# Kernel tuning notes

Measured on AMD Instinct MI355X. Metric: run time of the kernel, lower is better.

Reference implementation:

```python
import jax, jax.numpy as jnp
import numpy as np

CHUNK = 64
L2_EPS = 1e-6
RMS_EPS = 1e-5


def _silu(x):
    return x * jax.nn.sigmoid(x)


def _causal_shared_conv(x, w):
    # x: [B,T,C]; w: [K] single kernel shared across all channels (depthwise).
    K = w.shape[0]
    T = x.shape[1]
    xp = jnp.pad(x, ((0, 0), (K - 1, 0), (0, 0)))
    out = w[0] * xp[:, 0:T, :]
    for j in range(1, K):  # K=4, tiny fixed loop
        out = out + w[j] * xp[:, j:j + T, :]
    return out


def _l2norm(x):
    return x * jax.lax.rsqrt(jnp.sum(x * x, axis=-1, keepdims=True) + L2_EPS)


def _delta_rule_chunk(q, k, v, beta, chunk=CHUNK):
    # q,k: [B,H,T,dk]; v: [B,H,T,dv]; beta: [B,H,T]
    B, H, T, dk = q.shape
    dv = v.shape[-1]
    q = q * (dk ** -0.5)
    nC = T // chunk
    q = q.reshape(B, H, nC, chunk, dk)
    k = k.reshape(B, H, nC, chunk, dk)
    v = v.reshape(B, H, nC, chunk, dv)
    beta = beta.reshape(B, H, nC, chunk)
    k_beta = k * beta[..., None]
    v_beta = v * beta[..., None]
    # UT transform: invert the unit-lower-triangular (I + stril(K_beta K^T))
    A = jnp.einsum('bhncd,bhnmd->bhncm', k_beta, k)  # [B,H,nC,C,C]
    stril = jnp.tril(jnp.ones((chunk, chunk), bool), -1)
    M = jnp.where(stril, A, 0.0) + jnp.eye(chunk, dtype=q.dtype)
    u = jax.scipy.linalg.solve_triangular(M, v_beta, lower=True)  # T @ (beta*v)
    w = jax.scipy.linalg.solve_triangular(M, k_beta, lower=True)  # T @ (beta*k)
    tril_incl = jnp.tril(jnp.ones((chunk, chunk), bool))

    def step(S, inp):
        q_i, k_i, u_i, w_i = inp  # [B,H,C,d*]
        u_i = u_i - jnp.einsum('bhcd,bhde->bhce', w_i, S)
        attn = jnp.where(tril_incl, jnp.einsum('bhcd,bhmd->bhcm', q_i, k_i), 0.0)
        o_i = jnp.einsum('bhcd,bhde->bhce', q_i, S) + jnp.einsum('bhcm,bhme->bhce', attn, u_i)
        S = S + jnp.einsum('bhcd,bhce->bhde', k_i, u_i)
        return S, o_i

    xs = tuple(jnp.moveaxis(t, 2, 0) for t in (q, k, u, w))
    S0 = jnp.zeros((B, H, dk, dv), q.dtype)
    _, o = jax.lax.scan(step, S0, xs)  # o: [nC,B,H,C,dv]
    return jnp.moveaxis(o, 0, 2).reshape(B, H, T, dv)


def setup_inputs() -> dict:
    key = jax.random.key(0)
    ks = jax.random.split(key, 10)
    B, T, D, H = 2, 4096, 2048, 16
    sc = 0.02
    return {
        'x': jax.random.normal(ks[0], (B, T, D), jnp.float32),
        'Wq': jax.random.normal(ks[1], (D, D), jnp.float32) * sc,
        'Wk': jax.random.normal(ks[2], (D, D), jnp.float32) * sc,
        'Wv': jax.random.normal(ks[3], (D, D), jnp.float32) * sc,
        'Wb': jax.random.normal(ks[4], (D, H), jnp.float32) * sc,
        'Wo': jax.random.normal(ks[5], (D, D), jnp.float32) * sc,
        'conv_q': jax.random.normal(ks[6], (4,), jnp.float32) * 0.5,
        'conv_k': jax.random.normal(ks[7], (4,), jnp.float32) * 0.5,
        'conv_v': jax.random.normal(ks[8], (4,), jnp.float32) * 0.5,
        'onorm_w': jnp.ones((D // H,), jnp.float32),
    }


def reference(x, Wq, Wk, Wv, Wb, Wo, conv_q, conv_k, conv_v, onorm_w):
    B, T, D = x.shape
    H = Wb.shape[1]
    dk = Wq.shape[1] // H
    dv = Wv.shape[1] // H
    # projections + shared-kernel causal short conv (silu activation)
    q = _silu(_causal_shared_conv(x @ Wq, conv_q))
    k = _silu(_causal_shared_conv(x @ Wk, conv_k))
    v = _silu(_causal_shared_conv(x @ Wv, conv_v))
    beta = jax.nn.sigmoid(x @ Wb)  # [B,T,H]
    # split heads -> [B,H,T,d]
    qh = _l2norm(q.reshape(B, T, H, dk)).transpose(0, 2, 1, 3)
    kh = _l2norm(k.reshape(B, T, H, dk)).transpose(0, 2, 1, 3)
    vh = v.reshape(B, T, H, dv).transpose(0, 2, 1, 3)
    o = _delta_rule_chunk(qh, kh, vh, beta.transpose(0, 2, 1))  # [B,H,T,dv]
    o = o.transpose(0, 2, 1, 3)  # [B,T,H,dv]
    # per-head RMSNorm over head_v_dim
    o = o * jax.lax.rsqrt(jnp.mean(o * o, axis=-1, keepdims=True) + RMS_EPS) * onorm_w
    return o.reshape(B, T, H * dv) @ Wo
```

## Files before the change

kernel.cpp:

```cpp
#include <hip/hip_runtime.h>
#include <math.h>

#define B_ 2
#define T_ 4096
#define D_ 2048
#define H_ 16
#define DK 128
#define DV 128
#define CH 64
#define M_ (B_ * T_)
#define NCH (T_ / CH)

typedef __attribute__((ext_vector_type(8))) short bfrag;
typedef __attribute__((ext_vector_type(4))) float ffrag;
typedef __attribute__((ext_vector_type(8))) unsigned short u16x8;
typedef unsigned short us;

#define MFMA __builtin_amdgcn_mfma_f32_16x16x32_bf16

__device__ inline us f2bf(float f) {
  union { float f; unsigned u; } v; v.f = f;
  unsigned r = v.u + 0x7fffu + ((v.u >> 16) & 1u);
  return (us)(r >> 16);
}
__device__ inline float bf2f(us u) {
  union { unsigned u; float f; } v; v.u = ((unsigned)u) << 16;
  return v.f;
}

__device__ inline void gl_lds16(const us* g, us* l) {
  __builtin_amdgcn_global_load_lds(
      (const __attribute__((address_space(1))) void*)g,
      (__attribute__((address_space(3))) void*)l, 16, 0, 0);
}

__global__ __launch_bounds__(256) void to_bf16(const float* __restrict__ in,
                                               us* __restrict__ out) {
  const size_t i = ((size_t)blockIdx.x * 256 + threadIdx.x) * 8;
  const float4 a = *reinterpret_cast<const float4*>(in + i);
  const float4 b = *reinterpret_cast<const float4*>(in + i + 4);
  ushort4 o0, o1;
  o0.x = f2bf(a.x); o0.y = f2bf(a.y); o0.z = f2bf(a.z); o0.w = f2bf(a.w);
  o1.x = f2bf(b.x); o1.y = f2bf(b.y); o1.z = f2bf(b.z); o1.w = f2bf(b.w);
  *reinterpret_cast<ushort4*>(out + i) = o0;
  *reinterpret_cast<ushort4*>(out + i + 4) = o1;
}

__global__ __launch_bounds__(256) void wtrans(const float* __restrict__ W,
                                              us* __restrict__ Wt) {
  __shared__ float tile[64][68];
  const int k0 = blockIdx.y * 64, n0 = blockIdx.x * 64;
  const int lr = threadIdx.x >> 4, lc = (threadIdx.x & 15) * 4;
#pragma unroll
  for (int p = 0; p < 4; ++p) {
    const int r = lr + p * 16;
    *reinterpret_cast<float4*>(&tile[r][lc]) =
        *reinterpret_cast<const float4*>(&W[(size_t)(k0 + r) * D_ + n0 + lc]);
  }
  __syncthreads();
#pragma unroll
  for (int p = 0; p < 4; ++p) {
    const int r = lr + p * 16;
    ushort4 o;
    o.x = f2bf(tile[lc + 0][r]); o.y = f2bf(tile[lc + 1][r]);
    o.z = f2bf(tile[lc + 2][r]); o.w = f2bf(tile[lc + 3][r]);
    *reinterpret_cast<ushort4*>(&Wt[(size_t)(n0 + r) * D_ + k0 + lc]) = o;
  }
}

template <bool OUTF32>
__global__ __launch_bounds__(512, 2) void gemm256(const us* __restrict__ A,
                                                  const us* __restrict__ Bt,
                                                  void* __restrict__ Cp,
                                                  int M, int N, int K) {
  __shared__ __align__(16) us lds[2][2][2][256 * 32];
  const int t = threadIdx.x, l = t & 63, w = t >> 6;
  const int wm = w >> 2, wn = w & 3;
  const int fr = l & 15, hi = l >> 4;
  const int sx = 8 * (hi ^ ((fr >> 1) & 3));

  const int m0 = blockIdx.y * 256;
  const int n0 = blockIdx.x * 256;

  const int srow = t >> 2;
  const int scol = 8 * ((t & 3) ^ ((t >> 3) & 3));
  const us* Ab = A + (size_t)(m0 + srow) * K + scol;
  const us* Bb = Bt + (size_t)(n0 + srow) * K + scol;

  ffrag acc[8][4];
#pragma unroll
  for (int mi = 0; mi < 8; ++mi)
#pragma unroll
    for (int ni = 0; ni < 4; ++ni)
#pragma unroll
      for (int e = 0; e < 4; ++e) acc[mi][ni][e] = 0.f;

#define STG_A(bf, kk, kt)                                                      \
  do {                                                                         \
    gl_lds16(Ab + (size_t)(kt) * 64 + (kk) * 32, &lds[bf][0][kk][t * 8]);      \
    gl_lds16(Ab + (size_t)128 * K + (size_t)(kt) * 64 + (kk) * 32,             \
             &lds[bf][0][kk][4096 + t * 8]);                                   \
  } while (0)
#define STG_B(bf, kk, kt)                                                      \
  do {                                                                         \
    gl_lds16(Bb + (size_t)(kt) * 64 + (kk) * 32, &lds[bf][1][kk][t * 8]);      \
    gl_lds16(Bb + (size_t)128 * K + (size_t)(kt) * 64 + (kk) * 32,             \
             &lds[bf][1][kk][4096 + t * 8]);                                   \
  } while (0)

  const int NT = K >> 6;
  STG_A(0, 0, 0); STG_B(0, 0, 0); STG_A(0, 1, 0); STG_B(0, 1, 0);
  asm volatile("s_waitcnt vmcnt(4)" ::: "memory");
  __builtin_amdgcn_s_barrier();
  __builtin_amdgcn_sched_barrier(0);

  const int arow = wm * 128 + fr;
  const int brow = wn * 64 + fr;

#pragma unroll 1
  for (int kt = 0; kt < NT; ++kt) {
    const int cur = kt & 1, oth = cur ^ 1;
    const bool pf = (kt + 1 < NT);
    bfrag af4[4], bf4[4];

    {
      const us* pa = &lds[cur][0][0][0];
      const us* pb = &lds[cur][1][0][0];
#pragma unroll
      for (int ni = 0; ni < 4; ++ni)
        bf4[ni] = *reinterpret_cast<const bfrag*>(pb + (brow + ni * 16) * 32 + sx);
#pragma unroll
      for (int mi = 0; mi < 4; ++mi)
        af4[mi] = *reinterpret_cast<const bfrag*>(pa + (arow + mi * 16) * 32 + sx);
      if (pf) STG_A(oth, 0, kt + 1);
      __builtin_amdgcn_s_setprio(1);
#pragma unroll
      for (int mi = 0; mi < 4; ++mi)
#pragma unroll
        for (int ni = 0; ni < 4; ++ni)
          acc[mi][ni] = MFMA(af4[mi], bf4[ni], acc[mi][ni], 0, 0, 0);
      __builtin_amdgcn_s_setprio(0);
#pragma unroll
      for (int mi = 0; mi < 4; ++mi)
        af4[mi] = *reinterpret_cast<const bfrag*>(pa + (arow + 64 + mi * 16) * 32 + sx);
      if (pf) STG_B(oth, 0, kt + 1);
      __builtin_amdgcn_s_setprio(1);
#pragma unroll
      for (int mi = 0; mi < 4; ++mi)
#pragma unroll
        for (int ni = 0; ni < 4; ++ni)
          acc[mi + 4][ni] = MFMA(af4[mi], bf4[ni], acc[mi + 4][ni], 0, 0, 0);
      __builtin_amdgcn_s_setprio(0);
    }
    if (pf) asm volatile("s_waitcnt vmcnt(4)" ::: "memory");
    else    asm volatile("s_waitcnt vmcnt(0)" ::: "memory");
    __builtin_amdgcn_s_barrier();
    __builtin_amdgcn_sched_barrier(0);

    {
      const us* pa = &lds[cur][0][1][0];
      const us* pb = &lds[cur][1][1][0];
#pragma unroll
      for (int ni = 0; ni < 4; ++ni)
        bf4[ni] = *reinterpret_cast<const bfrag*>(pb + (brow + ni * 16) * 32 + sx);
#pragma unroll
      for (int mi = 0; mi < 4; ++mi)
        af4[mi] = *reinterpret_cast<const bfrag*>(pa + (arow + mi * 16) * 32 + sx);
      if (pf) STG_A(oth, 1, kt + 1);
      __builtin_amdgcn_s_setprio(1);
#pragma unroll
      for (int mi = 0; mi < 4; ++mi)
#pragma unroll
        for (int ni = 0; ni < 4; ++ni)
          acc[mi][ni] = MFMA(af4[mi], bf4[ni], acc[mi][ni], 0, 0, 0);
      __builtin_amdgcn_s_setprio(0);
#pragma unroll
      for (int mi = 0; mi < 4; ++mi)
        af4[mi] = *reinterpret_cast<const bfrag*>(pa + (arow + 64 + mi * 16) * 32 + sx);
      if (pf) STG_B(oth, 1, kt + 1);
      __builtin_amdgcn_s_setprio(1);
#pragma unroll
      for (int mi = 0; mi < 4; ++mi)
#pragma unroll
        for (int ni = 0; ni < 4; ++ni)
          acc[mi + 4][ni] = MFMA(af4[mi], bf4[ni], acc[mi + 4][ni], 0, 0, 0);
      __builtin_amdgcn_s_setprio(0);
    }
    if (pf) asm volatile("s_waitcnt vmcnt(4)" ::: "memory");
    else    asm volatile("s_waitcnt vmcnt(0)" ::: "memory");
    __builtin_amdgcn_s_barrier();
    __builtin_amdgcn_sched_barrier(0);
  }
#undef STG_A
#undef STG_B

  const int crow = m0 + wm * 128 + hi * 4;
  const int ccol = n0 + wn * 64 + fr;
#pragma unroll
  for (int mi = 0; mi < 8; ++mi)
#pragma unroll
    for (int ni = 0; ni < 4; ++ni)
#pragma unroll
      for (int j = 0; j < 4; ++j) {
        const size_t idx = (size_t)(crow + mi * 16 + j) * N + ccol + ni * 16;
        if constexpr (OUTF32) ((float*)Cp)[idx] = acc[mi][ni][j];
        else ((us*)Cp)[idx] = f2bf(acc[mi][ni][j]);
      }
}

__device__ inline void conv_body(const us* __restrict__ in, const float* cw,
                                 int bt, int d0, int mode, float v[8]) {
  const int tb = bt & (T_ - 1);
  const us* row = in + (size_t)bt * D_ + d0;
#pragma unroll
  for (int j = 0; j < 8; ++j) v[j] = 0.f;
#pragma unroll
  for (int j = 0; j < 4; ++j) {
    if (tb >= j) {
      const us* rp = row - (size_t)(j * D_);
      const ushort4 a = *reinterpret_cast<const ushort4*>(rp);
      const ushort4 b = *reinterpret_cast<const ushort4*>(rp + 4);
      const float wj = cw[3 - j];
      v[0] = fmaf(wj, bf2f(a.x), v[0]); v[1] = fmaf(wj, bf2f(a.y), v[1]);
      v[2] = fmaf(wj, bf2f(a.z), v[2]); v[3] = fmaf(wj, bf2f(a.w), v[3]);
      v[4] = fmaf(wj, bf2f(b.x), v[4]); v[5] = fmaf(wj, bf2f(b.y), v[5]);
      v[6] = fmaf(wj, bf2f(b.z), v[6]); v[7] = fmaf(wj, bf2f(b.w), v[7]);
    }
  }
#pragma unroll
  for (int j = 0; j < 8; ++j) v[j] = v[j] / (1.f + expf(-v[j]));
  if (mode) {
    float ss = 0.f;
#pragma unroll
    for (int j = 0; j < 8; ++j) ss = fmaf(v[j], v[j], ss);
    ss += __shfl_xor(ss, 1);
    ss += __shfl_xor(ss, 2);
    ss += __shfl_xor(ss, 4);
    ss += __shfl_xor(ss, 8);
    float sc = rsqrtf(ss + 1e-6f);
    if (mode == 2) sc *= 0.08838834764831845f;
#pragma unroll
    for (int j = 0; j < 8; ++j) v[j] *= sc;
  }
}

__global__ __launch_bounds__(256) void conv_silu_plain(const us* __restrict__ in,
                                                       const float* __restrict__ cw,
                                                       us* __restrict__ out) {
  const int bt = blockIdx.x, d0 = threadIdx.x * 8;
  float v[8];
  conv_body(in, cw, bt, d0, 0, v);
  ushort4 o0, o1;
  o0.x = f2bf(v[0]); o0.y = f2bf(v[1]); o0.z = f2bf(v[2]); o0.w = f2bf(v[3]);
  o1.x = f2bf(v[4]); o1.y = f2bf(v[5]); o1.z = f2bf(v[6]); o1.w = f2bf(v[7]);
  us* op = out + (size_t)bt * D_ + d0;
  *reinterpret_cast<ushort4*>(op) = o0;
  *reinterpret_cast<ushort4*>(op + 4) = o1;
}

__global__ __launch_bounds__(256) void conv_silu_chunk(const us* __restrict__ in,
                                                       const float* __restrict__ cw,
                                                       us* __restrict__ out,
                                                       int mode) {
  const int bt = blockIdx.x, d0 = threadIdx.x * 8;
  float v[8];
  conv_body(in, cw, bt, d0, mode, v);
  const int b = bt >> 12, tt = bt & (T_ - 1);
  const int cid = tt >> 6, r = tt & 63;
  const int h = d0 >> 7, g = (d0 & 127) >> 3;
  us* dst = out + ((size_t)((b * H_ + h) * NCH + cid)) * (CH * DK) +
            r * 128 + ((g ^ (r & 15)) * 8);
  ushort4 o0, o1;
  o0.x = f2bf(v[0]); o0.y = f2bf(v[1]); o0.z = f2bf(v[2]); o0.w = f2bf(v[3]);
  o1.x = f2bf(v[4]); o1.y = f2bf(v[5]); o1.z = f2bf(v[6]); o1.w = f2bf(v[7]);
  *reinterpret_cast<ushort4*>(dst) = o0;
  *reinterpret_cast<ushort4*>(dst + 4) = o1;
}

__global__ __launch_bounds__(256) void beta_sigmoid(const float* __restrict__ x,
                                                    const float* __restrict__ Wb,
                                                    float* __restrict__ betaT) {
  const int t = threadIdx.x;
  const int m = blockIdx.x * 4 + (t >> 6);
  const int l = t & 63;
  const int c = l & 15;
  const int s = l >> 4;
  const float* xr = x + (size_t)m * D_;
  const int kb = s * (D_ / 4);
  float acc = 0.f;
  for (int k = 0; k < D_ / 4; ++k)
    acc = fmaf(xr[kb + k], Wb[(size_t)(kb + k) * H_ + c], acc);
  acc += __shfl_xor(acc, 16);
  acc += __shfl_xor(acc, 32);
  if (l < 16) {
    const int b = m >> 12, tt = m & (T_ - 1);
    betaT[((size_t)(b * H_ + c)) * T_ + tt] = 1.f / (1.f + expf(-acc));
  }
}

__device__ inline void prod_step(float* Tf, const float* Am, float* xbuf,
                                 int r, int c, int I, int J,
                                 int nk, int K0, int K1, int K2) {
  float X = 0.f;
  const int Ks[3] = {K0, K1, K2};
  for (int kk = 0; kk < nk; ++kk) {
    const int K = Ks[kk];
    const float* amrow = Am + (16 * I + r) * 72 + 16 * K;
    const float* tcol = Tf + (16 * K) * 68 + 16 * J + c;
#pragma unroll
    for (int m = 0; m < 16; ++m) X = fmaf(amrow[m], tcol[m * 68], X);
  }
  __syncthreads();
  xbuf[r * 17 + c] = X;
  __syncthreads();
  float s = 0.f;
  const float* trow = Tf + (16 * I + r) * 68 + 16 * I;
#pragma unroll
  for (int m = 0; m < 16; ++m) s = fmaf(trow[m], xbuf[m * 17 + c], s);
  Tf[(16 * I + r) * 68 + 16 * J + c] = -s;
  __syncthreads();
}

__global__ __launch_bounds__(256, 2) void delta_prep(const us* __restrict__ qch,
                                                     const us* __restrict__ kch,
                                                     const float* __restrict__ betaT,
                                                     us* __restrict__ v_uv,
                                                     us* __restrict__ Wout,
                                                     us* __restrict__ kTout,
                                                     us* __restrict__ Aout) {
  __shared__ __align__(16) unsigned char lds[72000];
  us*    ks    = (us*)(lds);
  us*    Tb    = (us*)(lds);
  float* Am    = (float*)(lds + 16384);
  us*    vTb   = (us*)(lds + 16384);
  float* Tf    = (float*)(lds + 34816);
  us*    atst  = (us*)(lds + 34816);
  us*    Wst   = (us*)(lds + 34816);
  us*    kTb   = (us*)(lds + 52224);
  us*    UVst  = (us*)(lds + 52224);
  float* betac = (float*)(lds + 70656);
  float* xbuf  = (float*)(lds + 70912);

  const int t = threadIdx.x, w = t >> 6, l = t & 63;
  const int rr = l & 15, hi = l >> 4;
  const int bx = blockIdx.x;
  const int bh = bx >> 6, cid = bx & 63;
  const int b = bh >> 4, h = bh & 15;
  const size_t rowbase = ((size_t)b * T_ + (size_t)cid * CH) * D_ + (size_t)h * DK;
  const size_t cbase = (size_t)bx * (CH * DK);
  const size_t abase = (size_t)bx * (CH * CH);

  {
    const us* kg = kch + cbase;
#pragma unroll
    for (int p = 0; p < 4; ++p)
      gl_lds16(kg + p * 2048 + t * 8, ks + p * 2048 + t * 8);
    const float4 z = make_float4(0.f, 0.f, 0.f, 0.f);
    *reinterpret_cast<float4*>(atst + t * 16) = z;
    *reinterpret_cast<float4*>(atst + t * 16 + 8) = z;
    if (t < 64) betac[t] = betaT[(size_t)bh * T_ + cid * CH + t];
  }
  __syncthreads();

  {
    bfrag qf[4], kf[4];
#pragma unroll
    for (int k4 = 0; k4 < 4; ++k4) {
      const int go = ((4 * k4 + hi) ^ rr) * 8;
      qf[k4] = *reinterpret_cast<const bfrag*>(qch + cbase + (16 * w + rr) * 128 + go);
      kf[k4] = *reinterpret_cast<const bfrag*>(ks + (16 * w + rr) * 128 + go);
    }
    for (int jt = 0; jt <= w; ++jt) {
      ffrag accA = {0.f, 0.f, 0.f, 0.f}, accQ = {0.f, 0.f, 0.f, 0.f};
#pragma unroll
      for (int k4 = 0; k4 < 4; ++k4) {
        const bfrag bfr = *reinterpret_cast<const bfrag*>(
            ks + (16 * jt + rr) * 128 + (((4 * k4 + hi) ^ rr) * 8));
        accA = MFMA(kf[k4], bfr, accA, 0, 0, 0);
        accQ = MFMA(qf[k4], bfr, accQ, 0, 0, 0);
      }
#pragma unroll
      for (int j4 = 0; j4 < 4; ++j4) {
        const int i = 16 * w + 4 * hi + j4, j = 16 * jt + rr;
        Am[i * 72 + j] = (j < i) ? betac[i] * accA[j4] : 0.f;
        if (j <= i)
          atst[i * 64 + (((j >> 3) ^ (i & 7)) * 8) + (j & 7)] = f2bf(accQ[j4]);
      }
    }
    const int r = t & 63, part = t >> 6;
#pragma unroll
    for (int gi = 0; gi < 4; ++gi) {
      const int g = 4 * part + gi;
      const u16x8 kv = *reinterpret_cast<const u16x8*>(ks + r * 128 + ((g ^ (r & 15)) * 8));
#pragma unroll
      for (int j = 0; j < 8; ++j) kTb[(g * 8 + j) * 72 + r] = kv[j];
    }
  }
  __syncthreads();

  {
#pragma unroll
    for (int p = 0; p < 2; ++p) {
      const int unit = t + p * 256;
      *reinterpret_cast<u16x8*>(Aout + abase + unit * 8) =
          *reinterpret_cast<const u16x8*>(atst + unit * 8);
    }
#pragma unroll
    for (int p = 0; p < 4; ++p) {
      const int unit = t + p * 256;
      const int d = unit >> 3, sg = unit & 7;
      *reinterpret_cast<u16x8*>(kTout + cbase + unit * 8) =
          *reinterpret_cast<const u16x8*>(kTb + d * 72 + ((sg ^ (d & 7)) * 8));
    }
  }
  __syncthreads();
  for (int i = t; i < 64 * 68; i += 256) Tf[i] = 0.f;
  __syncthreads();

  if (t < 64) {
    const int blk = t >> 4, j = t & 15, bd = blk * 16;
    Tf[(bd + j) * 68 + bd + j] = 1.f;
    for (int i = j + 1; i < 16; ++i) {
      float s = 0.f;
      for (int m = j; m < i; ++m)
        s = fmaf(Am[(bd + i) * 72 + bd + m], Tf[(bd + m) * 68 + bd + j], s);
      Tf[(bd + i) * 68 + bd + j] = -s;
    }
  }
  __syncthreads();

  {
    const int r = t >> 4, c = t & 15;
    prod_step(Tf, Am, xbuf, r, c, 1, 0, 1, 0, 0, 0);
    prod_step(Tf, Am, xbuf, r, c, 2, 0, 2, 0, 1, 0);
    prod_step(Tf, Am, xbuf, r, c, 3, 0, 3, 0, 1, 2);
    prod_step(Tf, Am, xbuf, r, c, 2, 1, 1, 1, 0, 0);
    prod_step(Tf, Am, xbuf, r, c, 3, 1, 2, 1, 2, 0);
    prod_step(Tf, Am, xbuf, r, c, 3, 2, 1, 2, 0, 0);
  }

  {
    const int vr = t >> 2, vp = t & 3;
    u16x8 vv[4];
#pragma unroll
    for (int g = 0; g < 4; ++g)
      vv[g] = *reinterpret_cast<const u16x8*>(v_uv + rowbase + (size_t)vr * D_ +
                                              vp * 32 + g * 8);
    const int ti = t >> 2, tg = t & 3;
    u16x8 w0, w1;
#pragma unroll
    for (int jj = 0; jj < 8; ++jj) {
      const int j0 = tg * 16 + jj, j1 = j0 + 8;
      w0[jj] = f2bf(Tf[ti * 68 + j0] * betac[j0]);
      w1[jj] = f2bf(Tf[ti * 68 + j1] * betac[j1]);
    }
    *reinterpret_cast<u16x8*>(Tb + ti * 72 + tg * 16) = w0;
    *reinterpret_cast<u16x8*>(Tb + ti * 72 + tg * 16 + 8) = w1;
#pragma unroll
    for (int g = 0; g < 4; ++g)
#pragma unroll
      for (int j = 0; j < 8; ++j)
        vTb[(vp * 32 + g * 8 + j) * 72 + vr] = vv[g][j];
  }
  __syncthreads();

  {
    bfrag ta[2];
#pragma unroll
    for (int k2 = 0; k2 < 2; ++k2)
      ta[k2] = *reinterpret_cast<const bfrag*>(Tb + (16 * w + rr) * 72 + 32 * k2 + 8 * hi);
#pragma unroll
    for (int dt = 0; dt < 8; ++dt) {
      ffrag acc = {0.f, 0.f, 0.f, 0.f};
#pragma unroll
      for (int k2 = 0; k2 < 2; ++k2) {
        const bfrag bfr = *reinterpret_cast<const bfrag*>(
            kTb + (16 * dt + rr) * 72 + 32 * k2 + 8 * hi);
        acc = MFMA(ta[k2], bfr, acc, 0, 0, 0);
      }
#pragma unroll
      for (int j4 = 0; j4 < 4; ++j4) {
        const int i = 16 * w + 4 * hi + j4, d = 16 * dt + rr;
        Wst[i * 128 + (((d >> 3) ^ (i & 15)) * 8) + (d & 7)] = f2bf(-acc[j4]);
      }
    }
  }
  __syncthreads();

  {
    bfrag ta[2];
#pragma unroll
    for (int k2 = 0; k2 < 2; ++k2)
      ta[k2] = *reinterpret_cast<const bfrag*>(Tb + (16 * w + rr) * 72 + 32 * k2 + 8 * hi);
#pragma unroll
    for (int et = 0; et < 8; ++et) {
      ffrag acc = {0.f, 0.f, 0.f, 0.f};
#pragma unroll
      for (int k2 = 0; k2 < 2; ++k2) {
        const bfrag bfr = *reinterpret_cast<const bfrag*>(
            vTb + (16 * et + rr) * 72 + 32 * k2 + 8 * hi);
        acc = MFMA(ta[k2], bfr, acc, 0, 0, 0);
      }
#pragma unroll
      for (int j4 = 0; j4 < 4; ++j4)
        UVst[(16 * w + 4 * hi + j4) * 128 + 16 * et + rr] = f2bf(acc[j4]);
    }
#pragma unroll
    for (int p = 0; p < 4; ++p) {
      const int unit = t + p * 256;
      *reinterpret_cast<u16x8*>(Wout + cbase + unit * 8) =
          *reinterpret_cast<const u16x8*>(Wst + unit * 8);
    }
  }
  __syncthreads();

#pragma unroll
  for (int p = 0; p < 4; ++p) {
    const int unit = t + p * 256;
    const int r = unit >> 4, g = unit & 15;
    *reinterpret_cast<u16x8*>(v_uv + rowbase + (size_t)r * D_ + g * 8) =
        *reinterpret_cast<const u16x8*>(UVst + r * 128 + g * 8);
  }
}

__global__ __launch_bounds__(256, 1) void delta_seq(const us* __restrict__ qch,
                                                    const us* __restrict__ Wch,
                                                    const us* __restrict__ kTch,
                                                    const us* __restrict__ atch,
                                                    us* __restrict__ uv_o) {
  __shared__ __align__(16) us qs[2][CH * DK];
  __shared__ __align__(16) us Ws[2][CH * DK];
  __shared__ __align__(16) us kTs[2][DK * CH];
  __shared__ __align__(16) us ats[2][CH * CH];
  __shared__ __align__(16) us uvs[2][CH * 16];
  __shared__ __align__(16) us Sb[2][16 * 136];
  __shared__ __align__(16) us ub[CH * 18];

  const int t = threadIdx.x, l = t & 63, w = t >> 6;
  const int bx = blockIdx.x;
  const int vs = bx >> 5, bh = bx & 31;
  const int b = bh >> 4, h = bh & 15;
  const int rr = l & 15, hi = l >> 4;

  ffrag sacc[2];
#pragma unroll
  for (int t2 = 0; t2 < 2; ++t2)
#pragma unroll
    for (int j = 0; j < 4; ++j) sacc[t2][j] = 0.f;

  for (int i = t; i < 16 * 136; i += 256) Sb[0][i] = 0;

  const size_t cbQ = (size_t)(bh * NCH) * (CH * DK);
  const size_t cbA = (size_t)(bh * NCH) * (CH * CH);
  const size_t rowbase0 = ((size_t)b * T_) * D_ + (size_t)h * DK + vs * 16;

#define STAGE(buf, cid)                                                        \
  do {                                                                         \
    const us* qg = qch + cbQ + (size_t)(cid) * (CH * DK);                      \
    const us* Wg = Wch + cbQ + (size_t)(cid) * (CH * DK);                      \
    const us* kg = kTch + cbQ + (size_t)(cid) * (CH * DK);                     \
    const us* ag = atch + cbA + (size_t)(cid) * (CH * CH);                     \
    _Pragma("unroll")                                                          \
    for (int p = 0; p < 4; ++p) {                                              \
      gl_lds16(qg + p * 2048 + t * 8, &qs[buf][p * 2048 + t * 8]);             \
      gl_lds16(Wg + p * 2048 + t * 8, &Ws[buf][p * 2048 + t * 8]);             \
      gl_lds16(kg + p * 2048 + t * 8, &kTs[buf][p * 2048 + t * 8]);            \
    }                                                                          \
    _Pragma("unroll")                                                          \
    for (int p = 0; p < 2; ++p)                                                \
      gl_lds16(ag + p * 2048 + t * 8, &ats[buf][p * 2048 + t * 8]);            \
    if (t < 128)                                                               \
      gl_lds16(uv_o + rowbase0 + (size_t)((cid) * CH + (t >> 1)) * D_ + (t & 1) * 8, \
               &uvs[buf][t * 8]);                                              \
  } while (0)

  STAGE(0, 0);
  asm volatile("s_waitcnt vmcnt(0) lgkmcnt(0)" ::: "memory");
  __builtin_amdgcn_s_barrier();
  __builtin_amdgcn_sched_barrier(0);

  for (int cid = 0; cid < NCH; ++cid) {
    const int cur = cid & 1;
    if (cid + 1 < NCH) STAGE(cur ^ 1, cid + 1);

    bfrag sbf[4];
#pragma unroll
    for (int ks = 0; ks < 4; ++ks)
      sbf[ks] = *reinterpret_cast<const bfrag*>(&Sb[cur][rr * 136 + ks * 32 + hi * 8]);

    {
      ffrag uacc;
#pragma unroll
      for (int j = 0; j < 4; ++j)
        uacc[j] = bf2f(uvs[cur][(16 * w + 4 * hi + j) * 16 + rr]);
#pragma unroll
      for (int ks = 0; ks < 4; ++ks) {
        const bfrag af = *reinterpret_cast<const bfrag*>(
            &Ws[cur][(16 * w + rr) * 128 + (((4 * ks + hi) ^ rr) * 8)]);
        uacc = MFMA(af, sbf[ks], uacc, 0, 0, 0);
      }
#pragma unroll
      for (int j = 0; j < 4; ++j)
        ub[(16 * w + 4 * hi + j) * 18 + rr] = f2bf(uacc[j]);
    }
    asm volatile("s_waitcnt lgkmcnt(0)" ::: "memory");
    __builtin_amdgcn_s_barrier();
    __builtin_amdgcn_sched_barrier(0);

    {
      ffrag oacc;
#pragma unroll
      for (int j = 0; j < 4; ++j) oacc[j] = 0.f;
#pragma unroll
      for (int ks = 0; ks < 4; ++ks) {
        const bfrag af = *reinterpret_cast<const bfrag*>(
            &qs[cur][(16 * w + rr) * 128 + (((4 * ks + hi) ^ rr) * 8)]);
        oacc = MFMA(af, sbf[ks], oacc, 0, 0, 0);
      }
      const int nks = (w < 2) ? 1 : 2;
      for (int ks = 0; ks < nks; ++ks) {
        bfrag ubf;
#pragma unroll
        for (int j = 0; j < 8; ++j)
          ubf[j] = (short)ub[(32 * ks + 8 * hi + j) * 18 + rr];
        const bfrag af = *reinterpret_cast<const bfrag*>(
            &ats[cur][(16 * w + rr) * 64 + (((4 * ks + hi) ^ (rr & 7)) * 8)]);
        oacc = MFMA(af, ubf, oacc, 0, 0, 0);
      }
      us* og = uv_o + rowbase0 + (size_t)(cid * CH) * D_;
#pragma unroll
      for (int j = 0; j < 4; ++j)
        og[(size_t)(16 * w + 4 * hi + j) * D_ + rr] = f2bf(oacc[j]);
    }

    {
      bfrag ubf[2];
#pragma unroll
      for (int ks = 0; ks < 2; ++ks)
#pragma unroll
        for (int j = 0; j < 8; ++j)
          ubf[ks][j] = (short)ub[(32 * ks + 8 * hi + j) * 18 + rr];
#pragma unroll
      for (int t2 = 0; t2 < 2; ++t2) {
        const int tile = 2 * w + t2;
#pragma unroll
        for (int ks = 0; ks < 2; ++ks) {
          const bfrag af = *reinterpret_cast<const bfrag*>(
              &kTs[cur][(16 * tile + rr) * 64 + (((4 * ks + hi) ^ (rr & 7)) * 8)]);
          sacc[t2] = MFMA(af, ubf[ks], sacc[t2], 0, 0, 0);
        }
        ushort4 sw;
        sw.x = f2bf(sacc[t2][0]); sw.y = f2bf(sacc[t2][1]);
        sw.z = f2bf(sacc[t2][2]); sw.w = f2bf(sacc[t2][3]);
        *reinterpret_cast<ushort4*>(&Sb[cur ^ 1][rr * 136 + 16 * tile + 4 * hi]) = sw;
      }
    }
    asm volatile("s_waitcnt vmcnt(0) lgkmcnt(0)" ::: "memory");
    __builtin_amdgcn_s_barrier();
    __builtin_amdgcn_sched_barrier(0);
  }
#undef STAGE
}

__global__ __launch_bounds__(256) void rms_onorm_bf16(const us* __restrict__ in,
                                                      const float* __restrict__ w,
                                                      us* __restrict__ out) {
  const int bt = blockIdx.x;
  const int d0 = threadIdx.x * 8;
  const us* p = in + (size_t)bt * D_ + d0;
  const ushort4 a = *reinterpret_cast<const ushort4*>(p);
  const ushort4 b = *reinterpret_cast<const ushort4*>(p + 4);
  float v[8] = {bf2f(a.x), bf2f(a.y), bf2f(a.z), bf2f(a.w),
                bf2f(b.x), bf2f(b.y), bf2f(b.z), bf2f(b.w)};
  float ss = 0.f;
#pragma unroll
  for (int j = 0; j < 8; ++j) ss = fmaf(v[j], v[j], ss);
  ss += __shfl_xor(ss, 1);
  ss += __shfl_xor(ss, 2);
  ss += __shfl_xor(ss, 4);
  ss += __shfl_xor(ss, 8);
  const float sc = rsqrtf(ss * (1.0f / 128.0f) + 1e-5f);
  const int hd = d0 & 127;
  ushort4 o0, o1;
  o0.x = f2bf(v[0] * sc * w[hd + 0]); o0.y = f2bf(v[1] * sc * w[hd + 1]);
  o0.z = f2bf(v[2] * sc * w[hd + 2]); o0.w = f2bf(v[3] * sc * w[hd + 3]);
  o1.x = f2bf(v[4] * sc * w[hd + 4]); o1.y = f2bf(v[5] * sc * w[hd + 5]);
  o1.z = f2bf(v[6] * sc * w[hd + 6]); o1.w = f2bf(v[7] * sc * w[hd + 7]);
  us* op = out + (size_t)bt * D_ + d0;
  *reinterpret_cast<ushort4*>(op) = o0;
  *reinterpret_cast<ushort4*>(op + 4) = o1;
}

extern "C" void kernel_launch(void* const* d_in, const int* in_sizes, int n_in,
                              void* d_out, int out_size, void* d_ws, size_t ws_size,
                              hipStream_t stream) {
  const float* x  = (const float*)d_in[0];
  const float* Wq = (const float*)d_in[1];
  const float* Wk = (const float*)d_in[2];
  const float* Wv = (const float*)d_in[3];
  const float* Wb = (const float*)d_in[4];
  const float* Wo = (const float*)d_in[5];
  const float* cq = (const float*)d_in[6];
  const float* ck = (const float*)d_in[7];
  const float* cv = (const float*)d_in[8];
  const float* ow = (const float*)d_in[9];
  float* out = (float*)d_out;

  const size_t NE = (size_t)M_ * D_;
  us* ws   = (us*)d_ws;
  us* gout = ws;
  us* qch  = ws + NE;
  us* kch  = ws + 2 * NE;
  us* Wch  = ws + 3 * NE;
  us* kTch = ws + 4 * NE;
  us* wt   = ws + 5 * NE;
  us* attb = gout;
  float* betaT = (float*)(gout + 12 * 1024 * 1024);
  us* xb = (us*)d_out;
  us* vb = xb + NE;

  dim3 gg(D_ / 256, M_ / 256);
  dim3 wg(D_ / 64, D_ / 64);

  to_bf16<<<NE / 2048, 256, 0, stream>>>(x, xb);

  wtrans<<<wg, 256, 0, stream>>>(Wv, wt);
  gemm256<false><<<gg, 512, 0, stream>>>(xb, wt, gout, M_, D_, D_);
  conv_silu_plain<<<M_, 256, 0, stream>>>(gout, cv, vb);

  wtrans<<<wg, 256, 0, stream>>>(Wq, wt);
  gemm256<false><<<gg, 512, 0, stream>>>(xb, wt, gout, M_, D_, D_);
  conv_silu_chunk<<<M_, 256, 0, stream>>>(gout, cq, qch, 2);

  wtrans<<<wg, 256, 0, stream>>>(Wk, wt);
  gemm256<false><<<gg, 512, 0, stream>>>(xb, wt, gout, M_, D_, D_);
  conv_silu_chunk<<<M_, 256, 0, stream>>>(gout, ck, kch, 1);

  beta_sigmoid<<<M_ / 4, 256, 0, stream>>>(x, Wb, betaT);

  delta_prep<<<32 * NCH, 256, 0, stream>>>(qch, kch, betaT, vb, Wch, kTch, attb);
  delta_seq<<<256, 256, 0, stream>>>(qch, Wch, kTch, attb, vb);

  rms_onorm_bf16<<<M_, 256, 0, stream>>>(vb, ow, kTch);

  wtrans<<<wg, 256, 0, stream>>>(Wo, wt);
  gemm256<true><<<gg, 512, 0, stream>>>(kTch, wt, out, M_, D_, D_);
}
```

Measured before the change: 650.9 us.

## Fuse beta projection into bf16 cast; split delta_seq across eight specialized waves

The x-to-bf16 cast kernel now also computes the beta projection and sigmoid per row with a shuffle and LDS reduction, so the separate beta_sigmoid kernel and its second read of x go away. The sequential delta-rule kernel grows from 256 to 512 threads. Four waves compute the u correction and the state update, while the other four compute the output (q·S plus the intra-chunk attention term). Output tiles are staged in LDS and written coalesced one iteration later, and the beta buffer moves to a separate workspace region so it no longer aliases gout.

```diff
diff --git a/kernel.cpp b/kernel.cpp
--- a/kernel.cpp
+++ b/kernel.cpp
@@ -34,16 +34,58 @@
       (__attribute__((address_space(3))) void*)l, 16, 0, 0);
 }
 
-__global__ __launch_bounds__(256) void to_bf16(const float* __restrict__ in,
-                                               us* __restrict__ out) {
-  const size_t i = ((size_t)blockIdx.x * 256 + threadIdx.x) * 8;
-  const float4 a = *reinterpret_cast<const float4*>(in + i);
-  const float4 b = *reinterpret_cast<const float4*>(in + i + 4);
+__global__ __launch_bounds__(256) void x_prep(const float* __restrict__ x,
+                                              const float* __restrict__ Wb,
+                                              us* __restrict__ xb,
+                                              float* __restrict__ betaT) {
+  __shared__ float red[4][16];
+  const int m = blockIdx.x, t = threadIdx.x;
+  const int lane = t & 63, w = t >> 6;
+  const int d0 = t * 8;
+  const float* xr = x + (size_t)m * D_ + d0;
+  float v[8];
+  *reinterpret_cast<float4*>(&v[0]) = *reinterpret_cast<const float4*>(xr);
+  *reinterpret_cast<float4*>(&v[4]) = *reinterpret_cast<const float4*>(xr + 4);
   ushort4 o0, o1;
-  o0.x = f2bf(a.x); o0.y = f2bf(a.y); o0.z = f2bf(a.z); o0.w = f2bf(a.w);
-  o1.x = f2bf(b.x); o1.y = f2bf(b.y); o1.z = f2bf(b.z); o1.w = f2bf(b.w);
-  *reinterpret_cast<ushort4*>(out + i) = o0;
-  *reinterpret_cast<ushort4*>(out + i + 4) = o1;
+  o0.x = f2bf(v[0]); o0.y = f2bf(v[1]); o0.z = f2bf(v[2]); o0.w = f2bf(v[3]);
+  o1.x = f2bf(v[4]); o1.y = f2bf(v[5]); o1.z = f2bf(v[6]); o1.w = f2bf(v[7]);
+  us* xo = xb + (size_t)m * D_ + d0;
+  *reinterpret_cast<ushort4*>(xo) = o0;
+  *reinterpret_cast<ushort4*>(xo + 4) = o1;
+
+  float p[16];
+#pragma unroll
+  for (int h = 0; h < 16; ++h) p[h] = 0.f;
+#pragma unroll
+  for (int j = 0; j < 8; ++j) {
+    const float* wr = Wb + (size_t)(d0 + j) * H_;
+    const float4 w0 = *reinterpret_cast<const float4*>(wr);
+    const float4 w1 = *reinterpret_cast<const float4*>(wr + 4);
+    const float4 w2 = *reinterpret_cast<const float4*>(wr + 8);
+    const float4 w3 = *reinterpret_cast<const float4*>(wr + 12);
+    const float xv = v[j];
+    p[0] = fmaf(xv, w0.x, p[0]);  p[1] = fmaf(xv, w0.y, p[1]);
+    p[2] = fmaf(xv, w0.z, p[2]);  p[3] = fmaf(xv, w0.w, p[3]);
+    p[4] = fmaf(xv, w1.x, p[4]);  p[5] = fmaf(xv, w1.y, p[5]);
+    p[6] = fmaf(xv, w1.z, p[6]);  p[7] = fmaf(xv, w1.w, p[7]);
+    p[8] = fmaf(xv, w2.x, p[8]);  p[9] = fmaf(xv, w2.y, p[9]);
+    p[10] = fmaf(xv, w2.z, p[10]); p[11] = fmaf(xv, w2.w, p[11]);
+    p[12] = fmaf(xv, w3.x, p[12]); p[13] = fmaf(xv, w3.y, p[13]);
+    p[14] = fmaf(xv, w3.z, p[14]); p[15] = fmaf(xv, w3.w, p[15]);
+  }
+#pragma unroll
+  for (int off = 1; off < 64; off <<= 1)
+#pragma unroll
+    for (int h = 0; h < 16; ++h) p[h] += __shfl_xor(p[h], off);
+  if (lane == 0)
+#pragma unroll
+    for (int h = 0; h < 16; ++h) red[w][h] = p[h];
+  __syncthreads();
+  if (t < 16) {
+    const float s = red[0][t] + red[1][t] + red[2][t] + red[3][t];
+    const int b = m >> 12, tt = m & (T_ - 1);
+    betaT[((size_t)(b * H_ + t)) * T_ + tt] = 1.f / (1.f + expf(-s));
+  }
 }
 
 __global__ __launch_bounds__(256) void wtrans(const float* __restrict__ W,
@@ -275,27 +317,6 @@
   o1.x = f2bf(v[4]); o1.y = f2bf(v[5]); o1.z = f2bf(v[6]); o1.w = f2bf(v[7]);
   *reinterpret_cast<ushort4*>(dst) = o0;
   *reinterpret_cast<ushort4*>(dst + 4) = o1;
-}
-
-__global__ __launch_bounds__(256) void beta_sigmoid(const float* __restrict__ x,
-                                                    const float* __restrict__ Wb,
-                                                    float* __restrict__ betaT) {
-  const int t = threadIdx.x;
-  const int m = blockIdx.x * 4 + (t >> 6);
-  const int l = t & 63;
-  const int c = l & 15;
-  const int s = l >> 4;
-  const float* xr = x + (size_t)m * D_;
-  const int kb = s * (D_ / 4);
-  float acc = 0.f;
-  for (int k = 0; k < D_ / 4; ++k)
-    acc = fmaf(xr[kb + k], Wb[(size_t)(kb + k) * H_ + c], acc);
-  acc += __shfl_xor(acc, 16);
-  acc += __shfl_xor(acc, 32);
-  if (l < 16) {
-    const int b = m >> 12, tt = m & (T_ - 1);
-    betaT[((size_t)(b * H_ + c)) * T_ + tt] = 1.f / (1.f + expf(-acc));
-  }
 }
 
 __device__ inline void prod_step(float* Tf, const float* Am, float* xbuf,
@@ -523,7 +544,7 @@
   }
 }
 
-__global__ __launch_bounds__(256, 1) void delta_seq(const us* __restrict__ qch,
+__global__ __launch_bounds__(512, 1) void delta_seq(const us* __restrict__ qch,
                                                     const us* __restrict__ Wch,
                                                     const us* __restrict__ kTch,
                                                     const us* __restrict__ atch,
@@ -535,12 +556,14 @@
   __shared__ __align__(16) us uvs[2][CH * 16];
   __shared__ __align__(16) us Sb[2][16 * 136];
   __shared__ __align__(16) us ub[CH * 18];
+  __shared__ __align__(16) us ob[CH * 18];
 
   const int t = threadIdx.x, l = t & 63, w = t >> 6;
   const int bx = blockIdx.x;
   const int vs = bx >> 5, bh = bx & 31;
   const int b = bh >> 4, h = bh & 15;
   const int rr = l & 15, hi = l >> 4;
+  const int w2 = w & 3;
 
   ffrag sacc[2];
 #pragma unroll
@@ -548,7 +571,7 @@
 #pragma unroll
     for (int j = 0; j < 4; ++j) sacc[t2][j] = 0.f;
 
-  for (int i = t; i < 16 * 136; i += 256) Sb[0][i] = 0;
+  for (int i = t; i < 16 * 136; i += 512) Sb[0][i] = 0;
 
   const size_t cbQ = (size_t)(bh * NCH) * (CH * DK);
   const size_t cbA = (size_t)(bh * NCH) * (CH * CH);
@@ -560,15 +583,13 @@
     const us* Wg = Wch + cbQ + (size_t)(cid) * (CH * DK);                      \
     const us* kg = kTch + cbQ + (size_t)(cid) * (CH * DK);                     \
     const us* ag = atch + cbA + (size_t)(cid) * (CH * CH);                     \
-    _Pragma("unroll")                                                          \
-    for (int p = 0; p < 4; ++p) {                                              \
-      gl_lds16(qg + p * 2048 + t * 8, &qs[buf][p * 2048 + t * 8]);             \
-      gl_lds16(Wg + p * 2048 + t * 8, &Ws[buf][p * 2048 + t * 8]);             \
-      gl_lds16(kg + p * 2048 + t * 8, &kTs[buf][p * 2048 + t * 8]);            \
-    }                                                                          \
-    _Pragma("unroll")                                                          \
-    for (int p = 0; p < 2; ++p)                                                \
-      gl_lds16(ag + p * 2048 + t * 8, &ats[buf][p * 2048 + t * 8]);            \
+    gl_lds16(qg + t * 8, &qs[buf][t * 8]);                                     \
+    gl_lds16(qg + 4096 + t * 8, &qs[buf][4096 + t * 8]);                       \
+    gl_lds16(Wg + t * 8, &Ws[buf][t * 8]);                                     \
+    gl_lds16(Wg + 4096 + t * 8, &Ws[buf][4096 + t * 8]);                       \
+    gl_lds16(kg + t * 8, &kTs[buf][t * 8]);                                    \
+    gl_lds16(kg + 4096 + t * 8, &kTs[buf][4096 + t * 8]);                      \
+    gl_lds16(ag + t * 8, &ats[buf][t * 8]);                                    \
     if (t < 128)                                                               \
       gl_lds16(uv_o + rowbase0 + (size_t)((cid) * CH + (t >> 1)) * D_ + (t & 1) * 8, \
                &uvs[buf][t * 8]);                                              \
@@ -581,6 +602,12 @@
 
   for (int cid = 0; cid < NCH; ++cid) {
     const int cur = cid & 1;
+
+    if (cid > 0 && t < 128) {
+      const u16x8 ov = *reinterpret_cast<const u16x8*>(&ob[(t >> 1) * 18 + (t & 1) * 8]);
+      *reinterpret_cast<u16x8*>(uv_o + rowbase0 +
+          (size_t)((cid - 1) * CH + (t >> 1)) * D_ + (t & 1) * 8) = ov;
+    }
     if (cid + 1 < NCH) STAGE(cur ^ 1, cid + 1);
 
     bfrag sbf[4];
@@ -588,52 +615,35 @@
     for (int ks = 0; ks < 4; ++ks)
       sbf[ks] = *reinterpret_cast<const bfrag*>(&Sb[cur][rr * 136 + ks * 32 + hi * 8]);
 
-    {
-      ffrag uacc;
+    ffrag acc4;
+    if (w < 4) {
 #pragma unroll
       for (int j = 0; j < 4; ++j)
-        uacc[j] = bf2f(uvs[cur][(16 * w + 4 * hi + j) * 16 + rr]);
+        acc4[j] = bf2f(uvs[cur][(16 * w + 4 * hi + j) * 16 + rr]);
 #pragma unroll
       for (int ks = 0; ks < 4; ++ks) {
         const bfrag af = *reinterpret_cast<const bfrag*>(
             &Ws[cur][(16 * w + rr) * 128 + (((4 * ks + hi) ^ rr) * 8)]);
-        uacc = MFMA(af, sbf[ks], uacc, 0, 0, 0);
+        acc4 = MFMA(af, sbf[ks], acc4, 0, 0, 0);
       }
 #pragma unroll
       for (int j = 0; j < 4; ++j)
-        ub[(16 * w + 4 * hi + j) * 18 + rr] = f2bf(uacc[j]);
+        ub[(16 * w + 4 * hi + j) * 18 + rr] = f2bf(acc4[j]);
+    } else {
+#pragma unroll
+      for (int j = 0; j < 4; ++j) acc4[j] = 0.f;
+#pragma unroll
+      for (int ks = 0; ks < 4; ++ks) {
+        const bfrag af = *reinterpret_cast<const bfrag*>(
+            &qs[cur][(16 * w2 + rr) * 128 + (((4 * ks + hi) ^ rr) * 8)]);
+        acc4 = MFMA(af, sbf[ks], acc4, 0, 0, 0);
+      }
     }
     asm volatile("s_waitcnt lgkmcnt(0)" ::: "memory");
     __builtin_amdgcn_s_barrier();
     __builtin_amdgcn_sched_barrier(0);
 
-    {
-      ffrag oacc;
-#pragma unroll
-      for (int j = 0; j < 4; ++j) oacc[j] = 0.f;
-#pragma unroll
-      for (int ks = 0; ks < 4; ++ks) {
-        const bfrag af = *reinterpret_cast<const bfrag*>(
-            &qs[cur][(16 * w + rr) * 128 + (((4 * ks + hi) ^ rr) * 8)]);
-        oacc = MFMA(af, sbf[ks], oacc, 0, 0, 0);
-      }
-      const int nks = (w < 2) ? 1 : 2;
-      for (int ks = 0; ks < nks; ++ks) {
-        bfrag ubf;
-#pragma unroll
-        for (int j = 0; j < 8; ++j)
-          ubf[j] = (short)ub[(32 * ks + 8 * hi + j) * 18 + rr];
-        const bfrag af = *reinterpret_cast<const bfrag*>(
-            &ats[cur][(16 * w + rr) * 64 + (((4 * ks + hi) ^ (rr & 7)) * 8)]);
-        oacc = MFMA(af, ubf, oacc, 0, 0, 0);
-      }
-      us* og = uv_o + rowbase0 + (size_t)(cid * CH) * D_;
-#pragma unroll
-      for (int j = 0; j < 4; ++j)
-        og[(size_t)(16 * w + 4 * hi + j) * D_ + rr] = f2bf(oacc[j]);
-    }
-
-    {
+    if (w < 4) {
       bfrag ubf[2];
 #pragma unroll
       for (int ks = 0; ks < 2; ++ks)
@@ -654,12 +664,32 @@
         sw.z = f2bf(sacc[t2][2]); sw.w = f2bf(sacc[t2][3]);
         *reinterpret_cast<ushort4*>(&Sb[cur ^ 1][rr * 136 + 16 * tile + 4 * hi]) = sw;
       }
+    } else {
+      const int nks = (w2 < 2) ? 1 : 2;
+      for (int ks = 0; ks < nks; ++ks) {
+        bfrag ubf;
+#pragma unroll
+        for (int j = 0; j < 8; ++j)
+          ubf[j] = (short)ub[(32 * ks + 8 * hi + j) * 18 + rr];
+        const bfrag af = *reinterpret_cast<const bfrag*>(
+            &ats[cur][(16 * w2 + rr) * 64 + (((4 * ks + hi) ^ (rr & 7)) * 8)]);
+        acc4 = MFMA(af, ubf, acc4, 0, 0, 0);
+      }
+#pragma unroll
+      for (int j = 0; j < 4; ++j)
+        ob[(16 * w2 + 4 * hi + j) * 18 + rr] = f2bf(acc4[j]);
     }
     asm volatile("s_waitcnt vmcnt(0) lgkmcnt(0)" ::: "memory");
     __builtin_amdgcn_s_barrier();
     __builtin_amdgcn_sched_barrier(0);
   }
 #undef STAGE
+
+  if (t < 128) {
+    const u16x8 ov = *reinterpret_cast<const u16x8*>(&ob[(t >> 1) * 18 + (t & 1) * 8]);
+    *reinterpret_cast<u16x8*>(uv_o + rowbase0 +
+        (size_t)((NCH - 1) * CH + (t >> 1)) * D_ + (t & 1) * 8) = ov;
+  }
 }
 
 __global__ __launch_bounds__(256) void rms_onorm_bf16(const us* __restrict__ in,
@@ -715,14 +745,14 @@
   us* kTch = ws + 4 * NE;
   us* wt   = ws + 5 * NE;
   us* attb = gout;
-  float* betaT = (float*)(gout + 12 * 1024 * 1024);
+  float* betaT = (float*)(ws + 5 * NE + (size_t)D_ * D_);
   us* xb = (us*)d_out;
   us* vb = xb + NE;
 
   dim3 gg(D_ / 256, M_ / 256);
   dim3 wg(D_ / 64, D_ / 64);
 
-  to_bf16<<<NE / 2048, 256, 0, stream>>>(x, xb);
+  x_prep<<<M_, 256, 0, stream>>>(x, Wb, xb, betaT);
 
   wtrans<<<wg, 256, 0, stream>>>(Wv, wt);
   gemm256<false><<<gg, 512, 0, stream>>>(xb, wt, gout, M_, D_, D_);
@@ -736,10 +766,8 @@
   gemm256<false><<<gg, 512, 0, stream>>>(xb, wt, gout, M_, D_, D_);
   conv_silu_chunk<<<M_, 256, 0, stream>>>(gout, ck, kch, 1);
 
-  beta_sigmoid<<<M_ / 4, 256, 0, stream>>>(x, Wb, betaT);
-
   delta_prep<<<32 * NCH, 256, 0, stream>>>(qch, kch, betaT, vb, Wch, kTch, attb);
-  delta_seq<<<256, 256, 0, stream>>>(qch, Wch, kTch, attb, vb);
+  delta_seq<<<256, 512, 0, stream>>>(qch, Wch, kTch, attb, vb);
 
   rms_onorm_bf16<<<M_, 256, 0, stream>>>(vb, ow, kTch);
 
```

New measurement: 707.7 us. 8.7% more time.
